# Kernel tuning notes

Hardware: AMD Instinct MI355X
Metric: run time of the kernel (lower is better)

Reference implementation:

```python
import jax, jax.numpy as jnp
import numpy as np

DIM = 1024
N_HEADS = 16
HEAD_DIM = DIM // N_HEADS
MAX_SEQ_LEN = 8192
THETA = 10000.0
EPS = 1e-6


def _rope_tables(seq_len):
    freqs = 1.0 / (THETA ** (jnp.arange(0, HEAD_DIM, 2, dtype=jnp.float32) / HEAD_DIM))
    t = jnp.arange(seq_len, dtype=jnp.float32)
    ang = jnp.outer(t, freqs)  # [S, HEAD_DIM/2]
    return jnp.cos(ang), jnp.sin(ang)


def _apply_rope(x, cos, sin):
    # x: [B, H, S, hd]; cos/sin: [S, hd/2] broadcast over B,H
    x1 = x[..., ::2]
    x2 = x[..., 1::2]
    r1 = x1 * cos - x2 * sin
    r2 = x1 * sin + x2 * cos
    # interleave back: stack on last dim then flatten
    return jnp.stack([r1, r2], axis=-1).reshape(x.shape)


def _rms_norm(x, w, eps=EPS):
    dt = x.dtype
    xf = x.astype(jnp.float32)
    rms = jax.lax.rsqrt(jnp.mean(xf * xf, axis=-1, keepdims=True) + eps)
    return (xf * rms).astype(dt) * w.astype(dt)


def setup_inputs() -> dict:
    key = jax.random.key(0)
    ks = jax.random.split(key, 6)
    s = 0.02
    return {
        "x": jax.random.normal(ks[0], (2, 2048, DIM), dtype=jnp.float32),
        "Wq": jax.random.normal(ks[1], (DIM, DIM), dtype=jnp.float32) * s,
        "Wk": jax.random.normal(ks[2], (HEAD_DIM, DIM), dtype=jnp.float32) * s,
        "Wv": jax.random.normal(ks[3], (HEAD_DIM, DIM), dtype=jnp.float32) * s,
        "Wo": jax.random.normal(ks[4], (DIM, DIM), dtype=jnp.float32) * s,
        "norm_w": jnp.ones((DIM,), dtype=jnp.float32),
    }


def reference(x, Wq, Wk, Wv, Wo, norm_w):
    B, S, D = x.shape
    scale = HEAD_DIM ** -0.5
    # projections (nn.Linear: x @ W.T)
    q = (x @ Wq.T).reshape(B, S, N_HEADS, HEAD_DIM).transpose(0, 2, 1, 3)  # [B,H,S,hd]
    k = (x @ Wk.T).reshape(B, S, 1, HEAD_DIM).transpose(0, 2, 1, 3)       # [B,1,S,hd]
    v = (x @ Wv.T).reshape(B, S, 1, HEAD_DIM).transpose(0, 2, 1, 3)       # [B,1,S,hd]
    cos, sin = _rope_tables(S)
    q = _apply_rope(q, cos, sin)
    k = _apply_rope(k, cos, sin)
    # MQA: single KV head broadcast across query heads (keep k/v un-expanded)
    scores = jnp.einsum("bhqd,bzkd->bhqk", q, k) * scale  # [B,H,S,S]
    causal = jnp.tril(jnp.ones((S, S), dtype=bool))
    scores = jnp.where(causal, scores, jnp.finfo(scores.dtype).min)
    attn = jax.nn.softmax(scores, axis=-1)
    out = jnp.einsum("bhqk,bzkd->bhqd", attn, v)  # [B,H,S,hd]
    out = out.transpose(0, 2, 1, 3).reshape(B, S, D)
    out = _rms_norm(out, norm_w)
    return out @ Wo.T
```

## Files before the change

kernel.cpp:

```cpp
#include <hip/hip_runtime.h>
#include <hip/hip_bf16.h>

typedef __attribute__((ext_vector_type(4)))  float f32x4;
typedef __attribute__((ext_vector_type(16))) float f32x16;
typedef __attribute__((ext_vector_type(8)))  short s16x8;
typedef __attribute__((ext_vector_type(4)))  unsigned int u32x4;

using bf16 = __hip_bfloat16;

#define DIMC   1024
#define NH     16
#define HD     64
#define SEQ    2048
#define NB     2
#define NROWS  (NB*SEQ)
#define NQKV   1152
#define QSCL   0.18033688f

__global__ __launch_bounds__(256) void cast_all_kernel(const float* __restrict__ x,
                                                       const float* __restrict__ wq,
                                                       const float* __restrict__ wk,
                                                       const float* __restrict__ wv,
                                                       const float* __restrict__ wo,
                                                       const float* __restrict__ nw,
                                                       bf16* __restrict__ xbf,
                                                       bf16* __restrict__ wqkv,
                                                       bf16* __restrict__ wob) {
  int i = blockIdx.x * blockDim.x + threadIdx.x;
  if (i >= 1343488) {
    int j = i - 1343488;
    const float* s = wo + (size_t)j * 4;
    bf16* d = wob + (size_t)j * 4;
    int d0 = (j * 4) & 1023;
    float4 v = *(const float4*)s;
    float4 g = *(const float4*)(nw + d0);
    d[0] = __float2bfloat16(v.x * g.x);
    d[1] = __float2bfloat16(v.y * g.y);
    d[2] = __float2bfloat16(v.z * g.z);
    d[3] = __float2bfloat16(v.w * g.w);
    return;
  }
  const float* s;
  bf16* d;
  if (i < 1048576)      { s = x  + (size_t)i * 4;                 d = xbf + (size_t)i * 4; }
  else if (i < 1310720) { int j = i - 1048576; s = wq + (size_t)j * 4; d = wqkv + (size_t)j * 4; }
  else if (i < 1327104) { int j = i - 1310720; s = wk + (size_t)j * 4; d = wqkv + (size_t)1024 * 1024 + (size_t)j * 4; }
  else                  { int j = i - 1327104; s = wv + (size_t)j * 4; d = wqkv + (size_t)1088 * 1024 + (size_t)j * 4; }
  float4 v = *(const float4*)s;
  d[0] = __float2bfloat16(v.x);
  d[1] = __float2bfloat16(v.y);
  d[2] = __float2bfloat16(v.z);
  d[3] = __float2bfloat16(v.w);
}

template <bool SCALE, bool OUTBF>
__global__ __launch_bounds__(256) void gemm_bt(const bf16* __restrict__ A,
                                               const bf16* __restrict__ Bm,
                                               void* __restrict__ Cv,
                                               const float* __restrict__ ssq,
                                               int M, int N, int K) {
  __shared__ bf16 lA[128 * 64];
  __shared__ bf16 lB[64 * 64];
  __shared__ float rms_l[128];
  const int tid = threadIdx.x;
  const int w = tid >> 6, l = tid & 63;
  const int lg = l >> 4, ln = l & 15;
  const int wr = w >> 1, wc = w & 1;
  const int m0 = blockIdx.x * 128, n0 = blockIdx.y * 64;

  if (SCALE && tid < 128) {
    const float4* s4 = (const float4*)(ssq + (size_t)(m0 + tid) * 16);
    float4 a = s4[0], b = s4[1], c = s4[2], d = s4[3];
    float tot = (a.x + a.y + a.z + a.w) + (b.x + b.y + b.z + b.w) +
                (c.x + c.y + c.z + c.w) + (d.x + d.y + d.z + d.w);
    rms_l[tid] = rsqrtf(tot * (1.0f / 1024.0f) + 1e-6f);
  }

  f32x4 acc[4][2] = {};

  for (int k0 = 0; k0 < K; k0 += 64) {
#pragma unroll
    for (int it = 0; it < 4; ++it) {
      int c = tid + it * 256;
      int row = c >> 3, col = (c & 7) * 8;
      __builtin_amdgcn_global_load_lds(
          (const __attribute__((address_space(1))) void*)(A + (size_t)(m0 + row) * K + k0 + col),
          (__attribute__((address_space(3))) void*)(&lA[c * 8]), 16, 0, 0);
    }
#pragma unroll
    for (int it = 0; it < 2; ++it) {
      int c = tid + it * 256;
      int row = c >> 3, col = (c & 7) * 8;
      __builtin_amdgcn_global_load_lds(
          (const __attribute__((address_space(1))) void*)(Bm + (size_t)(n0 + row) * K + k0 + col),
          (__attribute__((address_space(3))) void*)(&lB[c * 8]), 16, 0, 0);
    }
    __syncthreads();
    for (int ks = 0; ks < 2; ++ks) {
      s16x8 af[4], bfr[2];
      for (int m = 0; m < 4; ++m)
        af[m] = *(const s16x8*)(&lA[(wr * 64 + m * 16 + ln) * 64 + ks * 32 + lg * 8]);
      for (int n = 0; n < 2; ++n)
        bfr[n] = *(const s16x8*)(&lB[(wc * 32 + n * 16 + ln) * 64 + ks * 32 + lg * 8]);
      for (int m = 0; m < 4; ++m)
        for (int n = 0; n < 2; ++n)
          acc[m][n] = __builtin_amdgcn_mfma_f32_16x16x32_bf16(af[m], bfr[n], acc[m][n], 0, 0, 0);
    }
    __syncthreads();
  }

  for (int m = 0; m < 4; ++m)
    for (int r = 0; r < 4; ++r) {
      int lrow = wr * 64 + m * 16 + lg * 4 + r;
      int grow = m0 + lrow;
      float sc = SCALE ? rms_l[lrow] : 1.0f;
      for (int n = 0; n < 2; ++n) {
        float v = SCALE ? acc[m][n][r] * sc : acc[m][n][r];
        size_t idx = (size_t)grow * N + n0 + wc * 32 + n * 16 + ln;
        if (OUTBF) ((bf16*)Cv)[idx] = __float2bfloat16(v);
        else       ((float*)Cv)[idx] = v;
      }
    }
}

__global__ __launch_bounds__(256) void rope_kernel(const bf16* __restrict__ Y,
                                                   bf16* __restrict__ QF,
                                                   bf16* __restrict__ KF,
                                                   bf16* __restrict__ VF) {
  const int r = blockIdx.x;
  const int b = r >> 11, s = r & 2047;
  const int qt = s >> 5, ql = s & 31;
  const bf16* y = Y + (size_t)r * NQKV;
  for (int t = threadIdx.x; t < 576; t += blockDim.x) {
    if (t < 512) {
      int h = t >> 5, i = t & 31;
      float x1 = __bfloat162float(y[h * 64 + 2 * i]);
      float x2 = __bfloat162float(y[h * 64 + 2 * i + 1]);
      float fr = expf(-(float)i * (9.210340371976184f / 32.0f));
      float sn, cs;
      sincosf((float)s * fr, &sn, &cs);
      int f = 2 * i;
      int ks = f >> 4, hi = (f >> 3) & 1, j = f & 7;
      bf16* q = QF + ((size_t)((((b * NH + h) * 64 + qt) * 4 + ks) * 64 + hi * 32 + ql)) * 8 + j;
      q[0] = __float2bfloat16((x1 * cs - x2 * sn) * QSCL);
      q[1] = __float2bfloat16((x1 * sn + x2 * cs) * QSCL);
    } else if (t < 544) {
      int i = t - 512;
      float x1 = __bfloat162float(y[1024 + 2 * i]);
      float x2 = __bfloat162float(y[1024 + 2 * i + 1]);
      float fr = expf(-(float)i * (9.210340371976184f / 32.0f));
      float sn, cs;
      sincosf((float)s * fr, &sn, &cs);
      int f = 2 * i;
      int ks = f >> 4, hi = (f >> 3) & 1, j = f & 7;
      bf16* k = KF + ((size_t)(((b * 64 + qt) * 4 + ks) * 64 + hi * 32 + ql)) * 8 + j;
      k[0] = __float2bfloat16(x1 * cs - x2 * sn);
      k[1] = __float2bfloat16(x1 * sn + x2 * cs);
    } else {
      int i = t - 544;
      int d0 = 2 * i;
      int c = (s >> 4) & 1, hv = (s >> 3) & 1, jv = s & 7;
      int dt = d0 >> 5;
      bf16* p0 = VF + ((size_t)((((b * 64 + qt) * 2 + c) * 2 + dt) * 64 + hv * 32 + (d0 & 31))) * 8 + jv;
      p0[0] = y[1088 + d0];
      p0[8] = y[1088 + d0 + 1];
    }
  }
}

static __device__ __forceinline__ unsigned cvt_pk_bf16(float lo, float hi) {
  unsigned r;
  asm("v_cvt_pk_bf16_f32 %0, %1, %2" : "=v"(r) : "v"(lo), "v"(hi));
  return r;
}
static __device__ __forceinline__ void pl32_swap(unsigned& x, unsigned& y) {
  asm("v_permlane32_swap_b32 %0, %1" : "+v"(x), "+v"(y));
}

__global__ __launch_bounds__(256) void attn11_kernel(const bf16* __restrict__ QF,
                                                     const bf16* __restrict__ KF,
                                                     const bf16* __restrict__ VF,
                                                     bf16* __restrict__ Nb,
                                                     float* __restrict__ ssq) {
  __shared__ float cb[2][64][33];
  const int bid = blockIdx.x;
  const int fold = bid >> 5;
  const int h  = (bid >> 1) & 15;
  const int b  = bid & 1;
  const int w  = threadIdx.x >> 6;
  const int l  = threadIdx.x & 63;
  const int ql = l & 31, hi = l >> 5;

  auto run_qtile = [&](int qt) {
    const bf16* qp = QF + ((size_t)((b * NH + h) * 64 + qt) * 4 * 64 + l) * 8;
    s16x8 qf[4];
#pragma unroll
    for (int ks = 0; ks < 4; ++ks)
      qf[ks] = *(const s16x8*)(qp + ks * 512);

    const bf16* kp = KF + ((size_t)(b * 64 + w) * 4 * 64 + l) * 8;
    const bf16* vp = VF + ((size_t)(b * 64 + w) * 4 * 64 + l) * 8;

    f32x16 ot[2] = {};
    float ls = 0.f;

    auto loadKV = [&](s16x8 (&kf)[4], s16x8 (&vf)[4]) {
#pragma unroll
      for (int ks = 0; ks < 4; ++ks) kf[ks] = *(const s16x8*)(kp + ks * 512);
#pragma unroll
      for (int j2 = 0; j2 < 4; ++j2) vf[j2] = *(const s16x8*)(vp + j2 * 512);
      kp += 4 * 2048;
      vp += 4 * 2048;
    };

    auto compute = [&](int t, s16x8 (&kf)[4], s16x8 (&vf)[4]) {
      f32x16 sa = {}, sb = {};
      __builtin_amdgcn_s_setprio(1);
      sa = __builtin_amdgcn_mfma_f32_32x32x16_bf16(kf[0], qf[0], sa, 0, 0, 0);
      sb = __builtin_amdgcn_mfma_f32_32x32x16_bf16(kf[2], qf[2], sb, 0, 0, 0);
      sa = __builtin_amdgcn_mfma_f32_32x32x16_bf16(kf[1], qf[1], sa, 0, 0, 0);
      sb = __builtin_amdgcn_mfma_f32_32x32x16_bf16(kf[3], qf[3], sb, 0, 0, 0);
      __builtin_amdgcn_s_setprio(0);

      float p[16];
      if (t == qt) {
#pragma unroll
        for (int r = 0; r < 16; ++r) {
          const int cr = (r & 3) + 8 * (r >> 2);
          p[r] = (cr + 4 * hi > ql) ? 0.f : exp2f(sa[r] + sb[r]);
        }
      } else {
#pragma unroll
        for (int r = 0; r < 16; ++r) p[r] = exp2f(sa[r] + sb[r]);
      }

      float t8[8];
#pragma unroll
      for (int r = 0; r < 8; ++r) t8[r] = p[2 * r] + p[2 * r + 1];
#pragma unroll
      for (int r = 0; r < 4; ++r) t8[r] = t8[r] + t8[r + 4];
      float rs = (t8[0] + t8[2]) + (t8[1] + t8[3]);
      rs += __shfl_xor(rs, 32);
      ls += rs;

      unsigned pw[8];
#pragma unroll
      for (int c = 0; c < 2; ++c) {
        unsigned w0 = cvt_pk_bf16(p[c * 8 + 0], p[c * 8 + 1]);
        unsigned w2 = cvt_pk_bf16(p[c * 8 + 4], p[c * 8 + 5]);
        unsigned w1 = cvt_pk_bf16(p[c * 8 + 2], p[c * 8 + 3]);
        unsigned w3 = cvt_pk_bf16(p[c * 8 + 6], p[c * 8 + 7]);
        pl32_swap(w0, w2);
        pl32_swap(w1, w3);
        pw[c * 4 + 0] = w0; pw[c * 4 + 1] = w1; pw[c * 4 + 2] = w2; pw[c * 4 + 3] = w3;
      }
      __builtin_amdgcn_s_setprio(1);
#pragma unroll
      for (int c = 0; c < 2; ++c) {
        u32x4 pu = {pw[c * 4 + 0], pw[c * 4 + 1], pw[c * 4 + 2], pw[c * 4 + 3]};
        s16x8 pb = *(s16x8*)&pu;
#pragma unroll
        for (int dt = 0; dt < 2; ++dt)
          ot[dt] = __builtin_amdgcn_mfma_f32_32x32x16_bf16(vf[c * 2 + dt], pb, ot[dt], 0, 0, 0);
      }
      __builtin_amdgcn_s_setprio(0);
    };

    s16x8 kA[4], vA[4], kB[4], vB[4];
    int t = w;
    if (t <= qt) {
      loadKV(kA, vA);
      while (true) {
        if (t + 4 <= qt) loadKV(kB, vB);
        compute(t, kA, vA);
        t += 4;
        if (t > qt) break;
        if (t + 4 <= qt) loadKV(kA, vA);
        compute(t, kB, vB);
        t += 4;
        if (t > qt) break;
      }
    }

    auto dumpLDS = [&](int slot) {
      float* dst = &cb[slot][l][0];
#pragma unroll
      for (int r = 0; r < 16; ++r) dst[r] = ot[0][r];
#pragma unroll
      for (int r = 0; r < 16; ++r) dst[16 + r] = ot[1][r];
      dst[32] = ls;
    };
    auto mergeLDS = [&](int slot) {
      const float* src = &cb[slot][l][0];
#pragma unroll
      for (int r = 0; r < 16; ++r) ot[0][r] += src[r];
#pragma unroll
      for (int r = 0; r < 16; ++r) ot[1][r] += src[16 + r];
      ls += src[32];
    };

    __syncthreads();
    if (w == 1) dumpLDS(0);
    if (w == 3) dumpLDS(1);
    __syncthreads();
    if (w == 0) mergeLDS(0);
    if (w == 2) mergeLDS(1);
    __syncthreads();
    if (w == 2) dumpLDS(0);
    __syncthreads();
    if (w == 0) {
      mergeLDS(0);
      float inv = 1.0f / ls;
      float sq = 0.f;
      const int rowg = b * SEQ + qt * 32 + ql;
      bf16* nb = Nb + (size_t)rowg * DIMC + h * HD;
#pragma unroll
      for (int dt = 0; dt < 2; ++dt)
#pragma unroll
        for (int rq = 0; rq < 4; ++rq) {
          float o0 = ot[dt][4 * rq + 0] * inv, o1 = ot[dt][4 * rq + 1] * inv;
          float o2 = ot[dt][4 * rq + 2] * inv, o3 = ot[dt][4 * rq + 3] * inv;
          sq += o0 * o0 + o1 * o1 + o2 * o2 + o3 * o3;
          uint2 pk = { cvt_pk_bf16(o0, o1), cvt_pk_bf16(o2, o3) };
          *(uint2*)(nb + dt * 32 + rq * 8 + 4 * hi) = pk;
        }
      sq += __shfl_xor(sq, 32);
      if (hi == 0) ssq[rowg * 16 + h] = sq;
    }
  };

  run_qtile(fold);
  run_qtile(63 - fold);
}

extern "C" void kernel_launch(void* const* d_in, const int* in_sizes, int n_in,
                              void* d_out, int out_size, void* d_ws, size_t ws_size,
                              hipStream_t stream) {
  const float* x      = (const float*)d_in[0];
  const float* Wq     = (const float*)d_in[1];
  const float* Wk     = (const float*)d_in[2];
  const float* Wv     = (const float*)d_in[3];
  const float* Wo     = (const float*)d_in[4];
  const float* norm_w = (const float*)d_in[5];

  size_t off = 0;
  auto alloc = [&](size_t bytes) {
    void* p = (char*)d_ws + off;
    off += (bytes + 255) & ~(size_t)255;
    return p;
  };
  bf16*  Xbf  = (bf16*)alloc((size_t)NROWS * DIMC * 2);
  bf16*  Wqkv = (bf16*)alloc((size_t)NQKV * DIMC * 2);
  bf16*  Wob  = (bf16*)alloc((size_t)DIMC * DIMC * 2);
  bf16*  Yb   = (bf16*)alloc((size_t)NROWS * NQKV * 2);
  bf16*  QF   = (bf16*)alloc((size_t)NB * NH * 64 * 4 * 64 * 8 * 2);
  bf16*  KF   = (bf16*)alloc((size_t)NB * 64 * 4 * 64 * 8 * 2);
  bf16*  VF   = (bf16*)alloc((size_t)NB * 64 * 4 * 64 * 8 * 2);
  bf16*  Nb   = (bf16*)alloc((size_t)NROWS * DIMC * 2);
  float* ssq  = (float*)alloc((size_t)NROWS * 16 * 4);

  cast_all_kernel<<<6272, 256, 0, stream>>>(x, Wq, Wk, Wv, Wo, norm_w, Xbf, Wqkv, Wob);

  gemm_bt<false, true><<<dim3(NROWS / 128, NQKV / 64), 256, 0, stream>>>(
      Xbf, Wqkv, Yb, nullptr, NROWS, NQKV, DIMC);

  rope_kernel<<<NROWS, 256, 0, stream>>>(Yb, QF, KF, VF);

  attn11_kernel<<<NB * NH * 32, 256, 0, stream>>>(QF, KF, VF, Nb, ssq);

  gemm_bt<true, false><<<dim3(NROWS / 128, DIMC / 64), 256, 0, stream>>>(
      Nb, Wob, (float*)d_out, ssq, NROWS, DIMC, DIMC);
}
```

Baseline: 110.0 us.

## Process two query heads per attention block to reuse shared K/V tiles

The attention kernel now handles two heads per block, so each K/V tile loaded from memory feeds the MFMAs of both heads under MQA. This halves the block count to 512 and cuts K/V global traffic per head. V loads move into the compute step instead of being double-buffered, and launch bounds request 2 blocks per CU. The cost is higher register pressure and fewer blocks for load balancing, and the V load latency is less hidden.

```diff
diff --git a/kernel.cpp b/kernel.cpp
--- a/kernel.cpp
+++ b/kernel.cpp
@@ -177,53 +177,47 @@
   asm("v_permlane32_swap_b32 %0, %1" : "+v"(x), "+v"(y));
 }
 
-__global__ __launch_bounds__(256) void attn11_kernel(const bf16* __restrict__ QF,
-                                                     const bf16* __restrict__ KF,
-                                                     const bf16* __restrict__ VF,
-                                                     bf16* __restrict__ Nb,
-                                                     float* __restrict__ ssq) {
-  __shared__ float cb[2][64][33];
+__global__ __launch_bounds__(256, 2) void attn12_kernel(const bf16* __restrict__ QF,
+                                                        const bf16* __restrict__ KF,
+                                                        const bf16* __restrict__ VF,
+                                                        bf16* __restrict__ Nb,
+                                                        float* __restrict__ ssq) {
+  __shared__ float cb[2][64][66];
   const int bid = blockIdx.x;
-  const int fold = bid >> 5;
-  const int h  = (bid >> 1) & 15;
+  const int fold = bid >> 4;
+  const int hp = (bid >> 1) & 7;
   const int b  = bid & 1;
   const int w  = threadIdx.x >> 6;
   const int l  = threadIdx.x & 63;
   const int ql = l & 31, hi = l >> 5;
+  const int h0 = hp * 2, h1 = hp * 2 + 1;
 
   auto run_qtile = [&](int qt) {
-    const bf16* qp = QF + ((size_t)((b * NH + h) * 64 + qt) * 4 * 64 + l) * 8;
-    s16x8 qf[4];
-#pragma unroll
-    for (int ks = 0; ks < 4; ++ks)
-      qf[ks] = *(const s16x8*)(qp + ks * 512);
-
-    const bf16* kp = KF + ((size_t)(b * 64 + w) * 4 * 64 + l) * 8;
-    const bf16* vp = VF + ((size_t)(b * 64 + w) * 4 * 64 + l) * 8;
-
-    f32x16 ot[2] = {};
-    float ls = 0.f;
-
-    auto loadKV = [&](s16x8 (&kf)[4], s16x8 (&vf)[4]) {
+    const bf16* qp0 = QF + ((size_t)((b * NH + h0) * 64 + qt) * 256 + l) * 8;
+    const bf16* qp1 = QF + ((size_t)((b * NH + h1) * 64 + qt) * 256 + l) * 8;
+    s16x8 qf0[4], qf1[4];
+#pragma unroll
+    for (int ks = 0; ks < 4; ++ks) {
+      qf0[ks] = *(const s16x8*)(qp0 + ks * 512);
+      qf1[ks] = *(const s16x8*)(qp1 + ks * 512);
+    }
+
+    const bf16* kp = KF + ((size_t)(b * 64 + w) * 256 + l) * 8;
+    const bf16* vp = VF + ((size_t)(b * 64 + w) * 256 + l) * 8;
+
+    f32x16 ot0[2] = {}, ot1[2] = {};
+    float ls0 = 0.f, ls1 = 0.f;
+
+    auto loadK = [&](s16x8 (&kf)[4]) {
 #pragma unroll
       for (int ks = 0; ks < 4; ++ks) kf[ks] = *(const s16x8*)(kp + ks * 512);
-#pragma unroll
-      for (int j2 = 0; j2 < 4; ++j2) vf[j2] = *(const s16x8*)(vp + j2 * 512);
-      kp += 4 * 2048;
-      vp += 4 * 2048;
+      kp += 4 * 1024 * 2;
     };
 
-    auto compute = [&](int t, s16x8 (&kf)[4], s16x8 (&vf)[4]) {
-      f32x16 sa = {}, sb = {};
-      __builtin_amdgcn_s_setprio(1);
-      sa = __builtin_amdgcn_mfma_f32_32x32x16_bf16(kf[0], qf[0], sa, 0, 0, 0);
-      sb = __builtin_amdgcn_mfma_f32_32x32x16_bf16(kf[2], qf[2], sb, 0, 0, 0);
-      sa = __builtin_amdgcn_mfma_f32_32x32x16_bf16(kf[1], qf[1], sa, 0, 0, 0);
-      sb = __builtin_amdgcn_mfma_f32_32x32x16_bf16(kf[3], qf[3], sb, 0, 0, 0);
-      __builtin_amdgcn_s_setprio(0);
-
+    auto softmax_pv = [&](const f32x16& sa, const f32x16& sb, bool diag,
+                          float& ls, f32x16 (&ot)[2], s16x8 (&vf)[4]) {
       float p[16];
-      if (t == qt) {
+      if (diag) {
 #pragma unroll
         for (int r = 0; r < 16; ++r) {
           const int cr = (r & 3) + 8 * (r >> 2);
@@ -233,7 +227,6 @@
 #pragma unroll
         for (int r = 0; r < 16; ++r) p[r] = exp2f(sa[r] + sb[r]);
       }
-
       float t8[8];
 #pragma unroll
       for (int r = 0; r < 8; ++r) t8[r] = p[2 * r] + p[2 * r + 1];
@@ -242,8 +235,6 @@
       float rs = (t8[0] + t8[2]) + (t8[1] + t8[3]);
       rs += __shfl_xor(rs, 32);
       ls += rs;
-
-      unsigned pw[8];
 #pragma unroll
       for (int c = 0; c < 2; ++c) {
         unsigned w0 = cvt_pk_bf16(p[c * 8 + 0], p[c * 8 + 1]);
@@ -252,31 +243,48 @@
         unsigned w3 = cvt_pk_bf16(p[c * 8 + 6], p[c * 8 + 7]);
         pl32_swap(w0, w2);
         pl32_swap(w1, w3);
-        pw[c * 4 + 0] = w0; pw[c * 4 + 1] = w1; pw[c * 4 + 2] = w2; pw[c * 4 + 3] = w3;
-      }
-      __builtin_amdgcn_s_setprio(1);
-#pragma unroll
-      for (int c = 0; c < 2; ++c) {
-        u32x4 pu = {pw[c * 4 + 0], pw[c * 4 + 1], pw[c * 4 + 2], pw[c * 4 + 3]};
+        u32x4 pu = {w0, w1, w2, w3};
         s16x8 pb = *(s16x8*)&pu;
+        __builtin_amdgcn_s_setprio(1);
 #pragma unroll
         for (int dt = 0; dt < 2; ++dt)
           ot[dt] = __builtin_amdgcn_mfma_f32_32x32x16_bf16(vf[c * 2 + dt], pb, ot[dt], 0, 0, 0);
-      }
+        __builtin_amdgcn_s_setprio(0);
+      }
+    };
+
+    auto compute = [&](int t, s16x8 (&kf)[4]) {
+      s16x8 vf[4];
+#pragma unroll
+      for (int j = 0; j < 4; ++j) vf[j] = *(const s16x8*)(vp + j * 512);
+      vp += 4 * 1024 * 2;
+      const bool diag = (t == qt);
+      f32x16 s0a = {}, s0b = {}, s1a = {}, s1b = {};
+      __builtin_amdgcn_s_setprio(1);
+      s0a = __builtin_amdgcn_mfma_f32_32x32x16_bf16(kf[0], qf0[0], s0a, 0, 0, 0);
+      s1a = __builtin_amdgcn_mfma_f32_32x32x16_bf16(kf[0], qf1[0], s1a, 0, 0, 0);
+      s0b = __builtin_amdgcn_mfma_f32_32x32x16_bf16(kf[2], qf0[2], s0b, 0, 0, 0);
+      s1b = __builtin_amdgcn_mfma_f32_32x32x16_bf16(kf[2], qf1[2], s1b, 0, 0, 0);
+      s0a = __builtin_amdgcn_mfma_f32_32x32x16_bf16(kf[1], qf0[1], s0a, 0, 0, 0);
+      s1a = __builtin_amdgcn_mfma_f32_32x32x16_bf16(kf[1], qf1[1], s1a, 0, 0, 0);
+      s0b = __builtin_amdgcn_mfma_f32_32x32x16_bf16(kf[3], qf0[3], s0b, 0, 0, 0);
+      s1b = __builtin_amdgcn_mfma_f32_32x32x16_bf16(kf[3], qf1[3], s1b, 0, 0, 0);
       __builtin_amdgcn_s_setprio(0);
+      softmax_pv(s0a, s0b, diag, ls0, ot0, vf);
+      softmax_pv(s1a, s1b, diag, ls1, ot1, vf);
     };
 
-    s16x8 kA[4], vA[4], kB[4], vB[4];
+    s16x8 kA[4], kB[4];
     int t = w;
     if (t <= qt) {
-      loadKV(kA, vA);
+      loadK(kA);
       while (true) {
-        if (t + 4 <= qt) loadKV(kB, vB);
-        compute(t, kA, vA);
+        if (t + 4 <= qt) loadK(kB);
+        compute(t, kA);
         t += 4;
         if (t > qt) break;
-        if (t + 4 <= qt) loadKV(kA, vA);
-        compute(t, kB, vB);
+        if (t + 4 <= qt) loadK(kA);
+        compute(t, kB);
         t += 4;
         if (t > qt) break;
       }
@@ -285,18 +293,24 @@
     auto dumpLDS = [&](int slot) {
       float* dst = &cb[slot][l][0];
 #pragma unroll
-      for (int r = 0; r < 16; ++r) dst[r] = ot[0][r];
-#pragma unroll
-      for (int r = 0; r < 16; ++r) dst[16 + r] = ot[1][r];
-      dst[32] = ls;
+      for (int r = 0; r < 16; ++r) {
+        dst[r]      = ot0[0][r];
+        dst[16 + r] = ot0[1][r];
+        dst[32 + r] = ot1[0][r];
+        dst[48 + r] = ot1[1][r];
+      }
+      dst[64] = ls0; dst[65] = ls1;
     };
     auto mergeLDS = [&](int slot) {
       const float* src = &cb[slot][l][0];
 #pragma unroll
-      for (int r = 0; r < 16; ++r) ot[0][r] += src[r];
-#pragma unroll
-      for (int r = 0; r < 16; ++r) ot[1][r] += src[16 + r];
-      ls += src[32];
+      for (int r = 0; r < 16; ++r) {
+        ot0[0][r] += src[r];
+        ot0[1][r] += src[16 + r];
+        ot1[0][r] += src[32 + r];
+        ot1[1][r] += src[48 + r];
+      }
+      ls0 += src[64]; ls1 += src[65];
     };
 
     __syncthreads();
@@ -310,22 +324,41 @@
     __syncthreads();
     if (w == 0) {
       mergeLDS(0);
-      float inv = 1.0f / ls;
-      float sq = 0.f;
       const int rowg = b * SEQ + qt * 32 + ql;
-      bf16* nb = Nb + (size_t)rowg * DIMC + h * HD;
-#pragma unroll
-      for (int dt = 0; dt < 2; ++dt)
-#pragma unroll
-        for (int rq = 0; rq < 4; ++rq) {
-          float o0 = ot[dt][4 * rq + 0] * inv, o1 = ot[dt][4 * rq + 1] * inv;
-          float o2 = ot[dt][4 * rq + 2] * inv, o3 = ot[dt][4 * rq + 3] * inv;
-          sq += o0 * o0 + o1 * o1 + o2 * o2 + o3 * o3;
-          uint2 pk = { cvt_pk_bf16(o0, o1), cvt_pk_bf16(o2, o3) };
-          *(uint2*)(nb + dt * 32 + rq * 8 + 4 * hi) = pk;
-        }
-      sq += __shfl_xor(sq, 32);
-      if (hi == 0) ssq[rowg * 16 + h] = sq;
+      {
+        float inv = 1.0f / ls0;
+        float sq = 0.f;
+        bf16* nb = Nb + (size_t)rowg * DIMC + h0 * HD;
+#pragma unroll
+        for (int dt = 0; dt < 2; ++dt)
+#pragma unroll
+          for (int rq = 0; rq < 4; ++rq) {
+            float o0 = ot0[dt][4 * rq + 0] * inv, o1 = ot0[dt][4 * rq + 1] * inv;
+            float o2 = ot0[dt][4 * rq + 2] * inv, o3 = ot0[dt][4 * rq + 3] * inv;
+            sq += o0 * o0 + o1 * o1 + o2 * o2 + o3 * o3;
+            uint2 pk = { cvt_pk_bf16(o0, o1), cvt_pk_bf16(o2, o3) };
+            *(uint2*)(nb + dt * 32 + rq * 8 + 4 * hi) = pk;
+          }
+        sq += __shfl_xor(sq, 32);
+        if (hi == 0) ssq[rowg * 16 + h0] = sq;
+      }
+      {
+        float inv = 1.0f / ls1;
+        float sq = 0.f;
+        bf16* nb = Nb + (size_t)rowg * DIMC + h1 * HD;
+#pragma unroll
+        for (int dt = 0; dt < 2; ++dt)
+#pragma unroll
+          for (int rq = 0; rq < 4; ++rq) {
+            float o0 = ot1[dt][4 * rq + 0] * inv, o1 = ot1[dt][4 * rq + 1] * inv;
+            float o2 = ot1[dt][4 * rq + 2] * inv, o3 = ot1[dt][4 * rq + 3] * inv;
+            sq += o0 * o0 + o1 * o1 + o2 * o2 + o3 * o3;
+            uint2 pk = { cvt_pk_bf16(o0, o1), cvt_pk_bf16(o2, o3) };
+            *(uint2*)(nb + dt * 32 + rq * 8 + 4 * hi) = pk;
+          }
+        sq += __shfl_xor(sq, 32);
+        if (hi == 0) ssq[rowg * 16 + h1] = sq;
+      }
     }
   };
 
@@ -366,7 +399,7 @@
 
   rope_kernel<<<NROWS, 256, 0, stream>>>(Yb, QF, KF, VF);
 
-  attn11_kernel<<<NB * NH * 32, 256, 0, stream>>>(QF, KF, VF, Nb, ssq);
+  attn12_kernel<<<NB * 8 * 32, 256, 0, stream>>>(QF, KF, VF, Nb, ssq);
 
   gemm_bt<true, false><<<dim3(NROWS / 128, DIMC / 64), 256, 0, stream>>>(
       Nb, Wob, (float*)d_out, ssq, NROWS, DIMC, DIMC);
```

Measured after the change: 102.2 us. 1.08x faster.
